# Performance work log

Hardware: AMD Instinct MI355X
Metric: run time of the kernel (lower is better)

The kernel has to match this reference:

```python
import jax, jax.numpy as jnp
import numpy as np

N, E = 50000, 800000
IN_FEATS, HIDDEN, HEADS, NUM_CLASSES, EDGE_FEAT = 64, 64, 4, 4, 2
D_HEAD = HIDDEN // HEADS


def _lin(key, fan_in, fan_out):
    k1, k2 = jax.random.split(key)
    s = 1.0 / np.sqrt(fan_in)
    W = jax.random.uniform(k1, (fan_in, fan_out), jnp.float32, -s, s)
    b = jax.random.uniform(k2, (fan_out,), jnp.float32, -s, s)
    return W, b


def setup_inputs() -> dict:
    key = jax.random.key(0)
    ks = jax.random.split(key, 10)
    x = jax.random.normal(ks[0], (N, IN_FEATS), jnp.float32)
    edge_index = jax.random.randint(ks[1], (2, E), 0, N, jnp.int32)
    edge_attr = jax.random.normal(ks[2], (E, EDGE_FEAT), jnp.float32)
    Wn, bn = _lin(ks[3], IN_FEATS, HIDDEN)
    We, be = _lin(ks[4], EDGE_FEAT, HIDDEN)
    Wq, bq = _lin(ks[5], HIDDEN, HIDDEN)
    Wk, bk = _lin(ks[6], HIDDEN, HIDDEN)
    Wv, bv = _lin(ks[7], HIDDEN, HIDDEN)
    Ws, bs = _lin(ks[8], HIDDEN, HIDDEN)   # lin_skip (root weight)
    Wf, bf = _lin(ks[9], HIDDEN, NUM_CLASSES)
    return {"x": x, "edge_index": edge_index, "edge_attr": edge_attr,
            "Wn": Wn, "bn": bn, "We": We, "be": be,
            "Wq": Wq, "bq": bq, "Wk": Wk, "bk": bk, "Wv": Wv, "bv": bv,
            "Ws": Ws, "bs": bs, "Wf": Wf, "bf": bf}


def _segment_softmax(logits, seg, num_segments):
    # logits: [E, H], seg: [E] destination node ids
    m = jax.ops.segment_max(logits, seg, num_segments=num_segments)  # [N, H]
    m = jnp.where(jnp.isfinite(m), m, 0.0)
    e = jnp.exp(logits - m[seg])
    s = jax.ops.segment_sum(e, seg, num_segments=num_segments)
    return e / (s[seg] + 1e-16)


def reference(x, edge_index, edge_attr, Wn, bn, We, be, Wq, bq, Wk, bk, Wv, bv, Ws, bs, Wf, bf):
    src, dst = edge_index[0], edge_index[1]
    h = x @ Wn + bn                                   # [N, HIDDEN]
    ea = (edge_attr @ We + be).reshape(E, HEADS, D_HEAD)
    q = (h @ Wq + bq).reshape(N, HEADS, D_HEAD)
    k = (h @ Wk + bk).reshape(N, HEADS, D_HEAD)
    v = (h @ Wv + bv).reshape(N, HEADS, D_HEAD)
    # per-edge attention logits (PyG flow source_to_target: query at dst, key at src)
    logits = jnp.einsum('ehd,ehd->eh', q[dst], k[src]) / np.sqrt(D_HEAD)
    alpha = _segment_softmax(logits, dst, N)          # [E, H]
    # edge_attr added to values (lin_edge is None since edge_dim not set)
    msg = (v[src] + ea) * alpha[:, :, None]           # [E, H, D]
    out = jax.ops.segment_sum(msg, dst, num_segments=N).reshape(N, HIDDEN)
    out = out + h @ Ws + bs                           # root/skip connection
    # dropout is identity in eval mode
    edge_out = out[src] + out[dst]                    # [E, HIDDEN]
    return edge_out @ Wf + bf                         # [E, NUM_CLASSES]
```

## Files before the change

kernel.cpp:

```cpp
#include <hip/hip_runtime.h>
#include <hip/hip_bf16.h>
#include <hip/hip_fp16.h>

#define N_NODES 50000
#define N_EDGES 800000
#define NB_T64 ((N_NODES + 63) / 64)
#define WT_BLOCKS 16
#define CAP 64

#define BIN_SHIFT 8
#define NBINS ((N_NODES + 255) / 256)
#define CAP_BIN 5120
#define EPB 2048
#define NB_BIN ((N_EDGES + EPB - 1) / EPB)

typedef unsigned short u16;
typedef unsigned int   u32;
typedef __attribute__((ext_vector_type(8))) short short8;
typedef __attribute__((ext_vector_type(4))) float f32x4;

__device__ __forceinline__ float bf2f(u16 u) {
    union { u32 i; float f; } z; z.i = ((u32)u) << 16; return z.f;
}
__device__ __forceinline__ u16 f2bf(float f) {
    union { float f; u32 i; } z; z.f = f;
    u32 x = z.i;
    u32 r = (x + 0x7fffu + ((x >> 16) & 1u)) >> 16;
    return (u16)r;
}
__device__ __forceinline__ float ldf(const void* p, size_t i, bool isbf) {
    return isbf ? bf2f(((const u16*)p)[i]) : ((const float*)p)[i];
}
__device__ __forceinline__ u16 ldbf(const void* p, size_t i, bool isbf) {
    return isbf ? ((const u16*)p)[i] : f2bf(((const float*)p)[i]);
}

#define WSB_COUNT 772

__global__ __launch_bounds__(256) void k_init(
    const void* __restrict__ Wn, const void* __restrict__ bn,
    const void* __restrict__ Wq, const void* __restrict__ bq,
    const void* __restrict__ Wk, const void* __restrict__ bk,
    const void* __restrict__ Wv, const void* __restrict__ bv,
    const void* __restrict__ Ws, const void* __restrict__ bs,
    const void* __restrict__ We, const void* __restrict__ be,
    const void* __restrict__ Wf, const void* __restrict__ bfv,
    const int* __restrict__ ei, const void* __restrict__ ea,
    u16* __restrict__ wsT, float* __restrict__ wsB,
    uint2* __restrict__ bins, u32* __restrict__ gcur,
    const int isbf)
{
    const int t = threadIdx.x, bid = blockIdx.x;
    if (bid >= WT_BLOCKS) {
        __shared__ u32 h[NBINS];
        __shared__ u32 off[NBINS];
        const int blk = bid - WT_BLOCKS;
        const int e0 = blk * EPB + t * 8;
        const bool vec = (e0 + 8 <= N_EDGES);
        int dv[8];
        if (vec) {
            const int4 a = *(const int4*)(ei + N_EDGES + e0);
            const int4 b = *(const int4*)(ei + N_EDGES + e0 + 4);
            dv[0] = a.x; dv[1] = a.y; dv[2] = a.z; dv[3] = a.w;
            dv[4] = b.x; dv[5] = b.y; dv[6] = b.z; dv[7] = b.w;
        } else {
            #pragma unroll
            for (int j = 0; j < 8; ++j)
                dv[j] = (e0 + j < N_EDGES) ? ei[N_EDGES + e0 + j] : -1;
        }
        if (t < NBINS) { h[t] = 0; off[t] = 0; }
        __syncthreads();
        #pragma unroll
        for (int j = 0; j < 8; ++j)
            if (dv[j] >= 0) atomicAdd(&h[dv[j] >> BIN_SHIFT], 1u);
        __syncthreads();
        if (t < NBINS && h[t] != 0) h[t] = atomicAdd(&gcur[t], h[t]);
        __syncthreads();
        int sv[8];
        if (vec) {
            const int4 a = *(const int4*)(ei + e0);
            const int4 b = *(const int4*)(ei + e0 + 4);
            sv[0] = a.x; sv[1] = a.y; sv[2] = a.z; sv[3] = a.w;
            sv[4] = b.x; sv[5] = b.y; sv[6] = b.z; sv[7] = b.w;
        } else {
            #pragma unroll
            for (int j = 0; j < 8; ++j)
                sv[j] = (e0 + j < N_EDGES) ? ei[e0 + j] : 0;
        }
        #pragma unroll
        for (int j = 0; j < 8; ++j) {
            if (dv[j] < 0) continue;
            const int e = e0 + j;
            float ea0, ea1;
            if (isbf) {
                const u32 w2 = ((const u32*)ea)[e];
                ea0 = bf2f((u16)(w2 & 0xffffu));
                ea1 = bf2f((u16)(w2 >> 16));
            } else {
                const float2 f2 = ((const float2*)ea)[e];
                ea0 = f2.x; ea1 = f2.y;
            }
            const __half2 hh = __floats2half2_rn(ea0, ea1);
            const int b = dv[j] >> BIN_SHIFT;
            const u32 rank = atomicAdd(&off[b], 1u);
            const u32 slot = h[b] + rank;
            if (slot < CAP_BIN) {
                uint2 r;
                r.x = (u32)sv[j] | ((u32)dv[j] << 16);
                r.y = *(const u32*)&hh;
                bins[(size_t)b * CAP_BIN + slot] = r;
            }
        }
        return;
    }

    const int i = bid * 256 + t;
    {
        const int kk = i >> 6, n = i & 63;
        const int o = n * 64 + kk;
        wsT[0 * 4096 + o] = ldbf(Wn, i, isbf);
        wsT[1 * 4096 + o] = ldbf(Wq, i, isbf);
        wsT[2 * 4096 + o] = ldbf(Wk, i, isbf);
        wsT[3 * 4096 + o] = ldbf(Wv, i, isbf);
        wsT[4 * 4096 + o] = ldbf(Ws, i, isbf);
    }
    if (bid == 0) {
        if (t < 64) {
            wsB[t]       = ldf(bn, t, isbf);
            wsB[64 + t]  = ldf(bq, t, isbf);
            wsB[128 + t] = ldf(bk, t, isbf);
            wsB[192 + t] = ldf(bv, t, isbf);
            wsB[256 + t] = ldf(bs, t, isbf);
            wsB[320 + t] = ldf(We, t, isbf);
            wsB[384 + t] = ldf(We, 64 + t, isbf);
            wsB[448 + t] = ldf(be, t, isbf);
        }
        wsB[512 + t] = ldf(Wf, t, isbf);
        if (t < 4) wsB[768 + t] = ldf(bfv, t, isbf);
    }
}

__global__ __launch_bounds__(512, 4) void k_bn(
    const void* __restrict__ x,
    const u16* __restrict__ wsT, const float* __restrict__ wsB,
    const uint2* __restrict__ bins, const u32* __restrict__ gcur,
    int* __restrict__ deg, uint2* __restrict__ rec,
    u16* __restrict__ qbf, u16* __restrict__ kbf, u16* __restrict__ vbf,
    u16* __restrict__ obf, const int isbf)
{
    __shared__ u16 xs[2 * 32 * 72];
    const int t = threadIdx.x, bid = blockIdx.x;

    if (bid < NBINS) {
        __shared__ u32 cnt[1 << BIN_SHIFT];
        const int lo = bid << BIN_SHIFT;
        const int rsz = (N_NODES - lo < (1 << BIN_SHIFT)) ? (N_NODES - lo)
                                                          : (1 << BIN_SHIFT);
        for (int i = t; i < (1 << BIN_SHIFT); i += 512) cnt[i] = 0;
        __syncthreads();
        int n = (int)gcur[bid];
        if (n > CAP_BIN) n = CAP_BIN;
        const uint2* bp = bins + (size_t)bid * CAP_BIN;
        for (int i = t; i < n; i += 512) {
            const uint2 r = bp[i];
            const u32 d = r.x >> 16;
            const u32 rank = atomicAdd(&cnt[d - (u32)lo], 1u) & (u32)(CAP - 1);
            uint2 o;
            o.x = r.x & 0xffffu;
            o.y = r.y;
            rec[((size_t)d << 6) + rank] = o;
        }
        __syncthreads();
        for (int i = t; i < rsz; i += 512) deg[lo + i] = (int)cnt[i];
        return;
    }

    const int tt = t & 255, half = t >> 8;
    const int w = tt >> 6, lane = tt & 63;
    const int l15 = lane & 15, quad = lane >> 4;
    const int base = (bid - NBINS) * 64 + half * 32;
    u16* xh = xs + half * (32 * 72);

    {
        const int m = tt >> 3, kc = tt & 7;
        const int node = base + m;
        short8 vd = {0, 0, 0, 0, 0, 0, 0, 0};
        if (node < N_NODES) {
            if (isbf) {
                vd = *(const short8*)((const u16*)x + (size_t)node * 64 + kc * 8);
            } else {
                const float4 f0 = *(const float4*)((const float*)x + (size_t)node * 64 + kc * 8);
                const float4 f1 = *(const float4*)((const float*)x + (size_t)node * 64 + kc * 8 + 4);
                vd[0] = f2bf(f0.x); vd[1] = f2bf(f0.y);
                vd[2] = f2bf(f0.z); vd[3] = f2bf(f0.w);
                vd[4] = f2bf(f1.x); vd[5] = f2bf(f1.y);
                vd[6] = f2bf(f1.z); vd[7] = f2bf(f1.w);
            }
        }
        *(short8*)(xh + m * 72 + kc * 8) = vd;
    }
    short8 b1[2][4];
    if (w < 2) {
        #pragma unroll
        for (int ks = 0; ks < 2; ++ks)
            #pragma unroll
            for (int nt = 0; nt < 4; ++nt)
                b1[ks][nt] = *(const short8*)(wsT + (nt * 16 + l15) * 64 + ks * 32 + quad * 8);
    }
    __syncthreads();

    if (w < 2) {
        f32x4 acc1[4];
        #pragma unroll
        for (int nt = 0; nt < 4; ++nt) acc1[nt] = (f32x4){0.f, 0.f, 0.f, 0.f};
        #pragma unroll
        for (int ks = 0; ks < 2; ++ks) {
            const short8 a = *(const short8*)(xh + (w * 16 + l15) * 72 + ks * 32 + quad * 8);
            #pragma unroll
            for (int nt = 0; nt < 4; ++nt)
                acc1[nt] = __builtin_amdgcn_mfma_f32_16x16x32_bf16(a, b1[ks][nt], acc1[nt], 0, 0, 0);
        }
        #pragma unroll
        for (int nt = 0; nt < 4; ++nt)
            #pragma unroll
            for (int r = 0; r < 4; ++r) {
                const int m = w * 16 + quad * 4 + r;
                const int col = nt * 16 + l15;
                xh[m * 72 + col] = f2bf(acc1[nt][r] + wsB[col]);
            }
    }
    short8 b2[2][4];
    {
        const u16* wt = wsT + (w + 1) * 4096;
        #pragma unroll
        for (int ks = 0; ks < 2; ++ks)
            #pragma unroll
            for (int nt = 0; nt < 4; ++nt)
                b2[ks][nt] = *(const short8*)(wt + (nt * 16 + l15) * 64 + ks * 32 + quad * 8);
    }
    __syncthreads();

    {
        f32x4 acc2[2][4];
        #pragma unroll
        for (int mt = 0; mt < 2; ++mt)
            #pragma unroll
            for (int nt = 0; nt < 4; ++nt) acc2[mt][nt] = (f32x4){0.f, 0.f, 0.f, 0.f};
        #pragma unroll
        for (int ks = 0; ks < 2; ++ks) {
            short8 a[2];
            #pragma unroll
            for (int mt = 0; mt < 2; ++mt)
                a[mt] = *(const short8*)(xh + (mt * 16 + l15) * 72 + ks * 32 + quad * 8);
            #pragma unroll
            for (int nt = 0; nt < 4; ++nt)
                #pragma unroll
                for (int mt = 0; mt < 2; ++mt)
                    acc2[mt][nt] = __builtin_amdgcn_mfma_f32_16x16x32_bf16(a[mt], b2[ks][nt], acc2[mt][nt], 0, 0, 0);
        }
        const float* bias = wsB + 64 + w * 64;
        u16* outp = (w == 0) ? qbf : (w == 1) ? kbf : (w == 2) ? vbf : obf;
        #pragma unroll
        for (int mt = 0; mt < 2; ++mt)
            #pragma unroll
            for (int nt = 0; nt < 4; ++nt)
                #pragma unroll
                for (int r = 0; r < 4; ++r) {
                    const int node = base + mt * 16 + quad * 4 + r;
                    if (node >= N_NODES) continue;
                    const int col = nt * 16 + l15;
                    outp[(size_t)node * 64 + col] = f2bf(acc2[mt][nt][r] + bias[col]);
                }
    }
}

__global__ __launch_bounds__(256) void k_agg(
    const int* __restrict__ deg,
    const uint2* __restrict__ rec,
    const u16* __restrict__ qbf, const u16* __restrict__ kbf,
    const u16* __restrict__ vbf, const u16* __restrict__ obf,
    const float* __restrict__ wsB,
    float4* __restrict__ y)
{
    const int wid = (blockIdx.x * 256 + threadIdx.x) >> 6;
    const int lane = threadIdx.x & 63;
    if (wid >= N_NODES) return;
    const int d = wid;
    const int lg = lane & 15;
    const float we0 = wsB[320 + lane];
    const float we1 = wsB[384 + lane];
    const float bef = wsB[448 + lane];
    const ushort4 q4u = *(const ushort4*)(qbf + (size_t)d * 64 + lg * 4);
    const float q0 = bf2f(q4u.x), q1 = bf2f(q4u.y);
    const float q2 = bf2f(q4u.z), q3 = bf2f(q4u.w);
    const float qf = bf2f(qbf[(size_t)d * 64 + lane]);
    const int sb = ((lane >> 4) << 2) + (lane & 3);
    const int beg = d << 6;
    int dg = deg[d];
    dg = (dg > CAP) ? CAP : dg;

    float den = 0.f, accv = 0.f, sa0 = 0.f, sa1 = 0.f;
    int j = 0;
    if (dg >= 4) {
        uint2 rn0 = rec[beg + 0], rn1 = rec[beg + 1];
        uint2 rn2 = rec[beg + 2], rn3 = rec[beg + 3];
        for (; j + 4 <= dg; j += 4) {
            const uint2 r0 = rn0, r1 = rn1, r2 = rn2, r3 = rn3;
            const int g = lane >> 4;
            const u32 smine = (g & 2) ? ((g & 1) ? r3.x : r2.x)
                                      : ((g & 1) ? r1.x : r0.x);
            const ushort4 k4 = *(const ushort4*)(kbf + (size_t)smine * 64 + lg * 4);
            const float v0 = bf2f(vbf[(size_t)(int)r0.x * 64 + lane]);
            const float v1 = bf2f(vbf[(size_t)(int)r1.x * 64 + lane]);
            const float v2 = bf2f(vbf[(size_t)(int)r2.x * 64 + lane]);
            const float v3 = bf2f(vbf[(size_t)(int)r3.x * 64 + lane]);
            const int nb = (j + 8 <= dg) ? (beg + j + 4) : (beg + j);
            rn0 = rec[nb + 0]; rn1 = rec[nb + 1];
            rn2 = rec[nb + 2]; rn3 = rec[nb + 3];
            float prod = q0 * bf2f(k4.x) + q1 * bf2f(k4.y)
                       + q2 * bf2f(k4.z) + q3 * bf2f(k4.w);
            prod += __shfl_xor(prod, 1, 64);
            prod += __shfl_xor(prod, 2, 64);
            const float ex = __expf(prod * 0.25f);
            const float ex0 = __shfl(ex, sb, 64);
            const float ex1 = __shfl(ex, 16 + sb, 64);
            const float ex2 = __shfl(ex, 32 + sb, 64);
            const float ex3 = __shfl(ex, 48 + sb, 64);
            const float2 ea0 = __half22float2(*(const __half2*)&r0.y);
            const float2 ea1 = __half22float2(*(const __half2*)&r1.y);
            const float2 ea2 = __half22float2(*(const __half2*)&r2.y);
            const float2 ea3 = __half22float2(*(const __half2*)&r3.y);
            den  += (ex0 + ex1) + (ex2 + ex3);
            accv += ex0 * v0 + ex1 * v1 + ex2 * v2 + ex3 * v3;
            sa0  += ex0 * ea0.x + ex1 * ea1.x + ex2 * ea2.x + ex3 * ea3.x;
            sa1  += ex0 * ea0.y + ex1 * ea1.y + ex2 * ea2.y + ex3 * ea3.y;
        }
    }
    for (; j < dg; ++j) {
        const uint2 r0 = rec[beg + j];
        const size_t srow = (size_t)(int)r0.x * 64 + lane;
        float prod = qf * bf2f(kbf[srow]);
        prod += __shfl_xor(prod, 1, 64);
        prod += __shfl_xor(prod, 2, 64);
        prod += __shfl_xor(prod, 4, 64);
        prod += __shfl_xor(prod, 8, 64);
        const float ex = __expf(prod * 0.25f);
        const float2 eaf = __half22float2(*(const __half2*)&r0.y);
        den  += ex;
        accv += ex * bf2f(vbf[srow]);
        sa0  += ex * eaf.x;
        sa1  += ex * eaf.y;
    }
    const float num = accv + we0 * sa0 + we1 * sa1 + bef * den;
    const float res = bf2f(obf[(size_t)d * 64 + lane]) + num / (den + 1e-16f);

    float y0 = res * wsB[512 + lane * 4 + 0];
    float y1 = res * wsB[512 + lane * 4 + 1];
    float y2 = res * wsB[512 + lane * 4 + 2];
    float y3 = res * wsB[512 + lane * 4 + 3];
    #pragma unroll
    for (int o = 1; o < 64; o <<= 1) {
        y0 += __shfl_xor(y0, o, 64);
        y1 += __shfl_xor(y1, o, 64);
        y2 += __shfl_xor(y2, o, 64);
        y3 += __shfl_xor(y3, o, 64);
    }
    if (lane == 0) {
        float4 yv;
        yv.x = y0 + 0.5f * wsB[768];
        yv.y = y1 + 0.5f * wsB[769];
        yv.z = y2 + 0.5f * wsB[770];
        yv.w = y3 + 0.5f * wsB[771];
        y[d] = yv;
    }
}

__global__ __launch_bounds__(256) void k_edgeout(
    const int* __restrict__ ei,
    const float4* __restrict__ y,
    void* __restrict__ out, const int isbf)
{
    const int idx = blockIdx.x * 256 + threadIdx.x;
    const int e0 = idx * 2;
    if (e0 >= N_EDGES) return;
    const int2 ss = *(const int2*)(ei + e0);
    const int2 dd = *(const int2*)(ei + N_EDGES + e0);
    const float4 ya = y[ss.x], yb = y[dd.x];
    const float4 yc = y[ss.y], yd = y[dd.y];
    const float a0 = ya.x + yb.x, a1 = ya.y + yb.y;
    const float a2 = ya.z + yb.z, a3 = ya.w + yb.w;
    const float c0 = yc.x + yd.x, c1 = yc.y + yd.y;
    const float c2 = yc.z + yd.z, c3 = yc.w + yd.w;
    if (isbf) {
        uint4 r;
        r.x = (u32)f2bf(a0) | ((u32)f2bf(a1) << 16);
        r.y = (u32)f2bf(a2) | ((u32)f2bf(a3) << 16);
        r.z = (u32)f2bf(c0) | ((u32)f2bf(c1) << 16);
        r.w = (u32)f2bf(c2) | ((u32)f2bf(c3) << 16);
        *(uint4*)((u16*)out + (size_t)e0 * 4) = r;
    } else {
        float4 r0; r0.x = a0; r0.y = a1; r0.z = a2; r0.w = a3;
        float4 r1; r1.x = c0; r1.y = c1; r1.z = c2; r1.w = c3;
        *(float4*)((float*)out + (size_t)e0 * 4) = r0;
        *(float4*)((float*)out + (size_t)e0 * 4 + 4) = r1;
    }
}

extern "C" void kernel_launch(void* const* d_in, const int* in_sizes, int n_in,
                              void* d_out, int out_size, void* d_ws, size_t ws_size,
                              hipStream_t stream)
{
    (void)n_in; (void)out_size; (void)ws_size;
    const void* x   = d_in[0];
    const int*  ei  = (const int*)d_in[1];
    const void* ea  = d_in[2];
    const void* Wn  = d_in[3];  const void* bn  = d_in[4];
    const void* We  = d_in[5];  const void* be  = d_in[6];
    const void* Wq  = d_in[7];  const void* bq  = d_in[8];
    const void* Wk  = d_in[9];  const void* bk  = d_in[10];
    const void* Wv  = d_in[11]; const void* bv  = d_in[12];
    const void* Ws_ = d_in[13]; const void* bs  = d_in[14];
    const void* Wf  = d_in[15]; const void* bfv = d_in[16];

    const int isbf = (in_sizes[0] == N_NODES * 64 * 2) ? 1 : 0;

    char*   wsp   = (char*)d_ws;
    uint2*  rec   = (uint2*)wsp;
    float4* y     = (float4*)(rec + (size_t)N_NODES * CAP);
    u16*    qbf   = (u16*)(y + N_NODES);
    u16*    kbf   = qbf + (size_t)N_NODES * 64;
    u16*    vbf   = kbf + (size_t)N_NODES * 64;
    u16*    obf   = vbf + (size_t)N_NODES * 64;
    u16*    wsT   = obf + (size_t)N_NODES * 64;
    float*  wsB   = (float*)(wsT + 5 * 4096);
    int*    deg   = (int*)(wsB + WSB_COUNT);
    uint2*  bins  = (uint2*)(deg + N_NODES);
    u32*    gcur  = (u32*)(bins + (size_t)NBINS * CAP_BIN);

    hipMemsetAsync(gcur, 0, NBINS * sizeof(u32), stream);
    k_init<<<WT_BLOCKS + NB_BIN, 256, 0, stream>>>(
        Wn, bn, Wq, bq, Wk, bk, Wv, bv, Ws_, bs, We, be, Wf, bfv, ei, ea,
        wsT, wsB, bins, gcur, isbf);
    k_bn<<<NBINS + NB_T64, 512, 0, stream>>>(x, wsT, wsB, bins, gcur,
                                             deg, rec, qbf, kbf, vbf, obf, isbf);
    k_agg<<<(N_NODES * 64 + 255) / 256, 256, 0, stream>>>(deg, rec, qbf, kbf,
                                                          vbf, obf, wsB, y);
    k_edgeout<<<(N_EDGES / 2 + 255) / 256, 256, 0, stream>>>(ei, y, d_out, isbf);
}
```

Measured before the change: 203.0 us.

## Split each wave into four edge groups with per-lane vectorized K/V gathers

Restructures the aggregation so each 16-lane group of a wave handles a different edge and each lane owns four feature columns. K and V rows are gathered as ushort4, replacing four scalar V loads per step and the exp broadcast shuffles. Partial sums are combined across groups with cross-group shuffles after the loop. The scalar tail loop is replaced by predication with a validity mask. The final projection is done on four columns per lane with a shorter reduction. This lowers the number of memory instructions and shuffles per edge, at the cost of idle lanes on the last partial group.

```diff
diff --git a/kernel.cpp b/kernel.cpp
--- a/kernel.cpp
+++ b/kernel.cpp
@@ -287,79 +287,80 @@
     if (wid >= N_NODES) return;
     const int d = wid;
     const int lg = lane & 15;
-    const float we0 = wsB[320 + lane];
-    const float we1 = wsB[384 + lane];
-    const float bef = wsB[448 + lane];
+    const int g  = lane >> 4;
+
     const ushort4 q4u = *(const ushort4*)(qbf + (size_t)d * 64 + lg * 4);
     const float q0 = bf2f(q4u.x), q1 = bf2f(q4u.y);
     const float q2 = bf2f(q4u.z), q3 = bf2f(q4u.w);
-    const float qf = bf2f(qbf[(size_t)d * 64 + lane]);
-    const int sb = ((lane >> 4) << 2) + (lane & 3);
+
     const int beg = d << 6;
     int dg = deg[d];
     dg = (dg > CAP) ? CAP : dg;
 
-    float den = 0.f, accv = 0.f, sa0 = 0.f, sa1 = 0.f;
-    int j = 0;
-    if (dg >= 4) {
-        uint2 rn0 = rec[beg + 0], rn1 = rec[beg + 1];
-        uint2 rn2 = rec[beg + 2], rn3 = rec[beg + 3];
-        for (; j + 4 <= dg; j += 4) {
-            const uint2 r0 = rn0, r1 = rn1, r2 = rn2, r3 = rn3;
-            const int g = lane >> 4;
-            const u32 smine = (g & 2) ? ((g & 1) ? r3.x : r2.x)
-                                      : ((g & 1) ? r1.x : r0.x);
-            const ushort4 k4 = *(const ushort4*)(kbf + (size_t)smine * 64 + lg * 4);
-            const float v0 = bf2f(vbf[(size_t)(int)r0.x * 64 + lane]);
-            const float v1 = bf2f(vbf[(size_t)(int)r1.x * 64 + lane]);
-            const float v2 = bf2f(vbf[(size_t)(int)r2.x * 64 + lane]);
-            const float v3 = bf2f(vbf[(size_t)(int)r3.x * 64 + lane]);
-            const int nb = (j + 8 <= dg) ? (beg + j + 4) : (beg + j);
-            rn0 = rec[nb + 0]; rn1 = rec[nb + 1];
-            rn2 = rec[nb + 2]; rn3 = rec[nb + 3];
+    float den = 0.f, sa0 = 0.f, sa1 = 0.f;
+    float av0 = 0.f, av1 = 0.f, av2 = 0.f, av3 = 0.f;
+
+    if (dg > 0) {
+        const u16* kp = kbf + lg * 4;
+        const u16* vp = vbf + lg * 4;
+        uint2 rn = rec[beg + g];
+        for (int j = 0; j < dg; j += 4) {
+            const uint2 r = rn;
+            const int nb = (j + 4 < dg) ? (beg + j + 4) : (beg + j);
+            rn = rec[nb + g];
+            const bool valid = (j + g) < dg;
+            const u32 rx = valid ? r.x : 0u;
+            const u32 ry = valid ? r.y : 0u;
+            const size_t off = (size_t)rx * 64;
+            const ushort4 k4 = *(const ushort4*)(kp + off);
+            const ushort4 v4 = *(const ushort4*)(vp + off);
             float prod = q0 * bf2f(k4.x) + q1 * bf2f(k4.y)
                        + q2 * bf2f(k4.z) + q3 * bf2f(k4.w);
             prod += __shfl_xor(prod, 1, 64);
             prod += __shfl_xor(prod, 2, 64);
-            const float ex = __expf(prod * 0.25f);
-            const float ex0 = __shfl(ex, sb, 64);
-            const float ex1 = __shfl(ex, 16 + sb, 64);
-            const float ex2 = __shfl(ex, 32 + sb, 64);
-            const float ex3 = __shfl(ex, 48 + sb, 64);
-            const float2 ea0 = __half22float2(*(const __half2*)&r0.y);
-            const float2 ea1 = __half22float2(*(const __half2*)&r1.y);
-            const float2 ea2 = __half22float2(*(const __half2*)&r2.y);
-            const float2 ea3 = __half22float2(*(const __half2*)&r3.y);
-            den  += (ex0 + ex1) + (ex2 + ex3);
-            accv += ex0 * v0 + ex1 * v1 + ex2 * v2 + ex3 * v3;
-            sa0  += ex0 * ea0.x + ex1 * ea1.x + ex2 * ea2.x + ex3 * ea3.x;
-            sa1  += ex0 * ea0.y + ex1 * ea1.y + ex2 * ea2.y + ex3 * ea3.y;
-        }
-    }
-    for (; j < dg; ++j) {
-        const uint2 r0 = rec[beg + j];
-        const size_t srow = (size_t)(int)r0.x * 64 + lane;
-        float prod = qf * bf2f(kbf[srow]);
-        prod += __shfl_xor(prod, 1, 64);
-        prod += __shfl_xor(prod, 2, 64);
-        prod += __shfl_xor(prod, 4, 64);
-        prod += __shfl_xor(prod, 8, 64);
-        const float ex = __expf(prod * 0.25f);
-        const float2 eaf = __half22float2(*(const __half2*)&r0.y);
-        den  += ex;
-        accv += ex * bf2f(vbf[srow]);
-        sa0  += ex * eaf.x;
-        sa1  += ex * eaf.y;
-    }
-    const float num = accv + we0 * sa0 + we1 * sa1 + bef * den;
-    const float res = bf2f(obf[(size_t)d * 64 + lane]) + num / (den + 1e-16f);
-
-    float y0 = res * wsB[512 + lane * 4 + 0];
-    float y1 = res * wsB[512 + lane * 4 + 1];
-    float y2 = res * wsB[512 + lane * 4 + 2];
-    float y3 = res * wsB[512 + lane * 4 + 3];
+            float ex = __expf(prod * 0.25f);
+            ex = valid ? ex : 0.f;
+            const float2 eaf = __half22float2(*(const __half2*)&ry);
+            den += ex;
+            sa0 += ex * eaf.x;
+            sa1 += ex * eaf.y;
+            av0 += ex * bf2f(v4.x);
+            av1 += ex * bf2f(v4.y);
+            av2 += ex * bf2f(v4.z);
+            av3 += ex * bf2f(v4.w);
+        }
+    }
     #pragma unroll
-    for (int o = 1; o < 64; o <<= 1) {
+    for (int o = 16; o < 64; o <<= 1) {
+        den += __shfl_xor(den, o, 64);
+        sa0 += __shfl_xor(sa0, o, 64);
+        sa1 += __shfl_xor(sa1, o, 64);
+        av0 += __shfl_xor(av0, o, 64);
+        av1 += __shfl_xor(av1, o, 64);
+        av2 += __shfl_xor(av2, o, 64);
+        av3 += __shfl_xor(av3, o, 64);
+    }
+
+    const float4 we04 = *(const float4*)(wsB + 320 + lg * 4);
+    const float4 we14 = *(const float4*)(wsB + 384 + lg * 4);
+    const float4 bef4 = *(const float4*)(wsB + 448 + lg * 4);
+    const ushort4 o4 = *(const ushort4*)(obf + (size_t)d * 64 + lg * 4);
+    const float rden = 1.0f / (den + 1e-16f);
+    const float res0 = bf2f(o4.x) + (av0 + we04.x * sa0 + we14.x * sa1 + bef4.x * den) * rden;
+    const float res1 = bf2f(o4.y) + (av1 + we04.y * sa0 + we14.y * sa1 + bef4.y * den) * rden;
+    const float res2 = bf2f(o4.z) + (av2 + we04.z * sa0 + we14.z * sa1 + bef4.z * den) * rden;
+    const float res3 = bf2f(o4.w) + (av3 + we04.w * sa0 + we14.w * sa1 + bef4.w * den) * rden;
+
+    const float4 wf0 = *(const float4*)(wsB + 512 + (lg * 4 + 0) * 4);
+    const float4 wf1 = *(const float4*)(wsB + 512 + (lg * 4 + 1) * 4);
+    const float4 wf2 = *(const float4*)(wsB + 512 + (lg * 4 + 2) * 4);
+    const float4 wf3 = *(const float4*)(wsB + 512 + (lg * 4 + 3) * 4);
+    float y0 = res0 * wf0.x + res1 * wf1.x + res2 * wf2.x + res3 * wf3.x;
+    float y1 = res0 * wf0.y + res1 * wf1.y + res2 * wf2.y + res3 * wf3.y;
+    float y2 = res0 * wf0.z + res1 * wf1.z + res2 * wf2.z + res3 * wf3.z;
+    float y3 = res0 * wf0.w + res1 * wf1.w + res2 * wf2.w + res3 * wf3.w;
+    #pragma unroll
+    for (int o = 1; o < 16; o <<= 1) {
         y0 += __shfl_xor(y0, o, 64);
         y1 += __shfl_xor(y1, o, 64);
         y2 += __shfl_xor(y2, o, 64);
```

Result: no change. 201.9 us (-0.6%).
